# Optimization experiments

Measured on AMD Instinct MI355X. Metric: run time of the kernel, lower is better.

Reference implementation:

```python
import jax, jax.numpy as jnp
import numpy as np

# dims
B, S, D, H, F = 4, 1024, 1024, 16, 4096
DH = D // H
THETA0 = 1.0   # base firing threshold of AdaptiveLIFNeuron
RHO = 0.9      # adaptation decay
EPS = 1e-5


def layer_norm(x, g, b):
    mu = jnp.mean(x, axis=-1, keepdims=True)
    var = jnp.mean((x - mu) ** 2, axis=-1, keepdims=True)
    return (x - mu) * jax.lax.rsqrt(var + EPS) * g + b


def spike(u):
    # Heaviside forward, sigmoid surrogate gradient (straight-through)
    sg = jax.nn.sigmoid(4.0 * u)
    hard = (u > 0).astype(u.dtype)
    return sg + jax.lax.stop_gradient(hard - sg)


def setup_inputs() -> dict:
    key = jax.random.key(0)
    ks = jax.random.split(key, 8)
    std = 0.02
    w = lambda k, shape: jax.random.normal(k, shape, jnp.float32) * std
    return {
        "x": jax.random.normal(ks[0], (B, S, D), jnp.float32),
        "Wq": w(ks[1], (D, D)), "bq": jnp.zeros((D,), jnp.float32),
        "Wk": w(ks[2], (D, D)), "bk": jnp.zeros((D,), jnp.float32),
        "Wv": w(ks[3], (D, D)), "bv": jnp.zeros((D,), jnp.float32),
        "Wo": w(ks[4], (D, D)), "bo": jnp.zeros((D,), jnp.float32),
        "g1": jnp.ones((D,), jnp.float32), "b1": jnp.zeros((D,), jnp.float32),
        "W1": w(ks[5], (D, F)), "bf1": jnp.zeros((F,), jnp.float32),
        "W2": w(ks[6], (F, D)), "bf2": jnp.zeros((D,), jnp.float32),
        "g2": jnp.ones((D,), jnp.float32), "b2": jnp.zeros((D,), jnp.float32),
        "decay": jnp.full((F,), 0.8, jnp.float32),  # per-feature membrane leak
        "beta": jnp.full((F,), 0.1, jnp.float32),   # per-feature threshold adaptation
    }


def reference(x, Wq, bq, Wk, bk, Wv, bv, Wo, bo, g1, b1, W1, bf1, W2, bf2, g2, b2, decay, beta):
    # --- causal multi-head self-attention (DSALayer) ---
    q = (x @ Wq + bq).reshape(B, S, H, DH)
    k = (x @ Wk + bk).reshape(B, S, H, DH)
    v = (x @ Wv + bv).reshape(B, S, H, DH)
    scores = jnp.einsum("bqhd,bkhd->bhqk", q, k) / np.sqrt(DH).astype(np.float32)
    causal = jnp.tril(jnp.ones((S, S), bool))
    scores = jnp.where(causal, scores, jnp.asarray(-1e9, scores.dtype))
    p = jax.nn.softmax(scores, axis=-1)
    attn = jnp.einsum("bhqk,bkhd->bqhd", p, v).reshape(B, S, D) @ Wo + bo
    h = layer_norm(x + attn, g1, b1)

    # --- feed-forward with per-timestep adaptive LIF recurrence ---
    ff = h @ W1 + bf1                      # [B, S, F]

    def step(carry, xt):
        vm, a = carry                      # membrane potential, adaptation
        vm = decay * vm + xt
        u = vm - (THETA0 + a)
        s = spike(u)
        vm = vm * (1.0 - s)                # hard reset on spike
        a = RHO * a + beta * s
        return (vm, a), s

    init = (jnp.zeros((B, F), x.dtype), jnp.zeros((B, F), x.dtype))
    _, spikes = jax.lax.scan(step, init, jnp.swapaxes(ff, 0, 1))  # scan over time
    spikes = jnp.swapaxes(spikes, 0, 1)    # [B, S, F]

    ff_out = spikes @ W2 + bf2
    return layer_norm(h + ff_out, g2, b2)
```

## Files before the change

### kernel.cpp

```cpp
#include <hip/hip_runtime.h>
#include <hip/hip_bf16.h>
#include <stdint.h>

#define Bsz 4
#define Ssz 1024
#define Dsz 1024
#define Hsz 16
#define Fsz 4096

typedef __hip_bfloat16 bf16;
typedef __attribute__((ext_vector_type(8))) short bf16x8;
typedef __attribute__((ext_vector_type(4))) float f32x4;

typedef __attribute__((address_space(1))) const void gvoid_t;
typedef __attribute__((address_space(3))) void svoid_t;

__device__ __forceinline__ void gload16(const bf16* g, bf16* l) {
    __builtin_amdgcn_global_load_lds((gvoid_t*)g, (svoid_t*)l, 16, 0, 0);
}

__global__ __launch_bounds__(256) void split_k(const float* __restrict__ src,
                                               bf16* __restrict__ hi,
                                               bf16* __restrict__ lo) {
    const int i = (blockIdx.x * 256 + threadIdx.x) * 4;
    const float4 v = *(const float4*)(src + i);
    float vv[4] = {v.x, v.y, v.z, v.w};
    #pragma unroll
    for (int u = 0; u < 4; ++u) {
        const bf16 h = __float2bfloat16(vv[u]);
        hi[i + u] = h;
        lo[i + u] = __float2bfloat16(vv[u] - __bfloat162float(h));
    }
}

__global__ __launch_bounds__(256) void split_scale_strided_k(const float* __restrict__ src,
                                                             int stride, int coloff,
                                                             bf16* __restrict__ hi,
                                                             bf16* __restrict__ lo,
                                                             float scale) {
    const int i = (blockIdx.x * 256 + threadIdx.x) * 4;
    const int r = i >> 10, c = i & 1023;
    const float4 v = *(const float4*)(src + (size_t)r * stride + coloff + c);
    float vv[4] = {v.x * scale, v.y * scale, v.z * scale, v.w * scale};
    #pragma unroll
    for (int u = 0; u < 4; ++u) {
        const bf16 h = __float2bfloat16(vv[u]);
        hi[i + u] = h;
        lo[i + u] = __float2bfloat16(vv[u] - __bfloat162float(h));
    }
}

__global__ __launch_bounds__(256) void transpose_split_k(const float* __restrict__ in,
                                                         bf16* __restrict__ hiT,
                                                         bf16* __restrict__ loT,
                                                         int R, int C) {
    __shared__ float tile[32][33];
    const int bx = blockIdx.x * 32, by = blockIdx.y * 32;
    const int tx = threadIdx.x, ty = threadIdx.y;
    #pragma unroll
    for (int i = 0; i < 32; i += 8)
        tile[ty + i][tx] = in[(size_t)(by + ty + i) * C + bx + tx];
    __syncthreads();
    #pragma unroll
    for (int i = 0; i < 32; i += 8) {
        const float v = tile[tx][ty + i];
        const bf16 h = __float2bfloat16(v);
        const size_t o = (size_t)(bx + ty + i) * R + by + tx;
        hiT[o] = h;
        loT[o] = __float2bfloat16(v - __bfloat162float(h));
    }
}

__global__ __launch_bounds__(256) void transpose_cast_k(const float* __restrict__ in,
                                                        bf16* __restrict__ outT,
                                                        int R, int C) {
    __shared__ float tile[32][33];
    const int bx = blockIdx.x * 32, by = blockIdx.y * 32;
    const int tx = threadIdx.x, ty = threadIdx.y;
    #pragma unroll
    for (int i = 0; i < 32; i += 8)
        tile[ty + i][tx] = in[(size_t)(by + ty + i) * C + bx + tx];
    __syncthreads();
    #pragma unroll
    for (int i = 0; i < 32; i += 8)
        outT[(size_t)(bx + ty + i) * R + by + tx] = __float2bfloat16(tile[tx][ty + i]);
}

__global__ __launch_bounds__(256) void transpose_split_v_k(const float* __restrict__ v,
                                                           int stride, int coloff,
                                                           bf16* __restrict__ hiT,
                                                           bf16* __restrict__ loT) {
    __shared__ float tile[32][33];
    const int s0 = blockIdx.x * 32;
    const int dr0 = blockIdx.y * 32;
    const int b = dr0 >> 10, h = (dr0 >> 6) & 15, d0 = dr0 & 63;
    const int tx = threadIdx.x, ty = threadIdx.y;
    #pragma unroll
    for (int i = 0; i < 32; i += 8)
        tile[ty + i][tx] =
            v[(size_t)(b * Ssz + s0 + ty + i) * stride + coloff + h * 64 + d0 + tx];
    __syncthreads();
    #pragma unroll
    for (int i = 0; i < 32; i += 8) {
        const float val = tile[tx][ty + i];
        const bf16 hh = __float2bfloat16(val);
        const size_t o = (size_t)(dr0 + ty + i) * Ssz + s0 + tx;
        hiT[o] = hh;
        loT[o] = __float2bfloat16(val - __bfloat162float(hh));
    }
}

__global__ __launch_bounds__(256) void gemm3_bt(const bf16* __restrict__ Ah,
                                                const bf16* __restrict__ Al,
                                                const bf16* __restrict__ Bh,
                                                const bf16* __restrict__ Bl,
                                                const float* __restrict__ bias,
                                                float* __restrict__ Cf,
                                                int M, int N, int K) {
    __shared__ alignas(16) bf16 Ash[128 * 32];
    __shared__ alignas(16) bf16 Asl[128 * 32];
    __shared__ alignas(16) bf16 Bsh[128 * 32];
    __shared__ alignas(16) bf16 Bsl[128 * 32];
    const int t = threadIdx.x;
    const int lane = t & 63, wv = t >> 6;
    const int mw = wv >> 1, nw = wv & 1;
    const int m0 = blockIdx.y * 128, n0 = blockIdx.x * 128;
    const int r16 = lane & 15, q8 = (lane >> 4) * 8;
    const int arow = t >> 2, acol = (t & 3) * 8;

    const bf16* gAh = Ah + (size_t)(m0 + arow) * K + acol;
    const bf16* gAl = Al + (size_t)(m0 + arow) * K + acol;
    const bf16* gBh = Bh + (size_t)(n0 + arow) * K + acol;
    const bf16* gBl = Bl + (size_t)(n0 + arow) * K + acol;
    const size_t rK64 = (size_t)64 * K;
    bf16* lAh = Ash + wv * 512;
    bf16* lAl = Asl + wv * 512;
    bf16* lBh = Bsh + wv * 512;
    bf16* lBl = Bsl + wv * 512;

    f32x4 acc[4][4] = {};

    for (int k0 = 0; k0 < K; k0 += 32) {
        __syncthreads();
        gload16(gAh + k0, lAh);  gload16(gAh + k0 + rK64, lAh + 2048);
        gload16(gAl + k0, lAl);  gload16(gAl + k0 + rK64, lAl + 2048);
        gload16(gBh + k0, lBh);  gload16(gBh + k0 + rK64, lBh + 2048);
        gload16(gBl + k0, lBl);  gload16(gBl + k0 + rK64, lBl + 2048);
        __syncthreads();

        bf16x8 ah[4], al[4], bh[4], bl[4];
        #pragma unroll
        for (int rt = 0; rt < 4; ++rt) {
            const int ro = (64 * mw + 16 * rt + r16) * 32 + q8;
            ah[rt] = *(const bf16x8*)(Ash + ro);
            al[rt] = *(const bf16x8*)(Asl + ro);
        }
        #pragma unroll
        for (int ct = 0; ct < 4; ++ct) {
            const int co = (64 * nw + 16 * ct + r16) * 32 + q8;
            bh[ct] = *(const bf16x8*)(Bsh + co);
            bl[ct] = *(const bf16x8*)(Bsl + co);
        }
        #pragma unroll
        for (int rt = 0; rt < 4; ++rt)
            #pragma unroll
            for (int ct = 0; ct < 4; ++ct) {
                acc[rt][ct] = __builtin_amdgcn_mfma_f32_16x16x32_bf16(ah[rt], bh[ct], acc[rt][ct], 0, 0, 0);
                acc[rt][ct] = __builtin_amdgcn_mfma_f32_16x16x32_bf16(ah[rt], bl[ct], acc[rt][ct], 0, 0, 0);
                acc[rt][ct] = __builtin_amdgcn_mfma_f32_16x16x32_bf16(al[rt], bh[ct], acc[rt][ct], 0, 0, 0);
            }
    }

    const int rowi = (lane >> 4) * 4;
    const int coli = lane & 15;
    #pragma unroll
    for (int ct = 0; ct < 4; ++ct) {
        const int col = n0 + 64 * nw + 16 * ct + coli;
        const float bv = bias[col];
        #pragma unroll
        for (int rt = 0; rt < 4; ++rt) {
            const int rowb = m0 + 64 * mw + 16 * rt + rowi;
            #pragma unroll
            for (int r = 0; r < 4; ++r)
                Cf[(size_t)(rowb + r) * N + col] = acc[rt][ct][r] + bv;
        }
    }
}

__global__ __launch_bounds__(256) void gemm1_bt(const bf16* __restrict__ A,
                                                const bf16* __restrict__ Bt,
                                                const float* __restrict__ bias,
                                                float* __restrict__ Cf,
                                                int M, int N, int K) {
    __shared__ alignas(16) bf16 As[128 * 32];
    __shared__ alignas(16) bf16 Bs[128 * 32];
    const int t = threadIdx.x;
    const int lane = t & 63, wv = t >> 6;
    const int mw = wv >> 1, nw = wv & 1;
    const int m0 = blockIdx.y * 128, n0 = blockIdx.x * 128;
    const int r16 = lane & 15, q8 = (lane >> 4) * 8;
    const int arow = t >> 2, acol = (t & 3) * 8;

    const bf16* gA = A + (size_t)(m0 + arow) * K + acol;
    const bf16* gB = Bt + (size_t)(n0 + arow) * K + acol;
    const size_t rK64 = (size_t)64 * K;
    bf16* lA = As + wv * 512;
    bf16* lB = Bs + wv * 512;

    f32x4 acc[4][4] = {};

    for (int k0 = 0; k0 < K; k0 += 32) {
        __syncthreads();
        gload16(gA + k0, lA);  gload16(gA + k0 + rK64, lA + 2048);
        gload16(gB + k0, lB);  gload16(gB + k0 + rK64, lB + 2048);
        __syncthreads();

        bf16x8 af[4], bf_[4];
        #pragma unroll
        for (int rt = 0; rt < 4; ++rt)
            af[rt] = *(const bf16x8*)(As + (64 * mw + 16 * rt + r16) * 32 + q8);
        #pragma unroll
        for (int ct = 0; ct < 4; ++ct)
            bf_[ct] = *(const bf16x8*)(Bs + (64 * nw + 16 * ct + r16) * 32 + q8);
        #pragma unroll
        for (int rt = 0; rt < 4; ++rt)
            #pragma unroll
            for (int ct = 0; ct < 4; ++ct)
                acc[rt][ct] = __builtin_amdgcn_mfma_f32_16x16x32_bf16(
                    af[rt], bf_[ct], acc[rt][ct], 0, 0, 0);
    }

    const int rowi = (lane >> 4) * 4;
    const int coli = lane & 15;
    #pragma unroll
    for (int ct = 0; ct < 4; ++ct) {
        const int col = n0 + 64 * nw + 16 * ct + coli;
        const float bv = bias[col];
        #pragma unroll
        for (int rt = 0; rt < 4; ++rt) {
            const int rowb = m0 + 64 * mw + 16 * rt + rowi;
            #pragma unroll
            for (int r = 0; r < 4; ++r)
                Cf[(size_t)(rowb + r) * N + col] = acc[rt][ct][r] + bv;
        }
    }
}

__global__ __launch_bounds__(256) void attn_mfma_k(const bf16* __restrict__ qhp,
                                                   const bf16* __restrict__ qlp,
                                                   const bf16* __restrict__ khp,
                                                   const bf16* __restrict__ klp,
                                                   const bf16* __restrict__ vhp,
                                                   const bf16* __restrict__ vlp,
                                                   bf16* __restrict__ ohi,
                                                   bf16* __restrict__ olo) {
    __shared__ alignas(16) bf16 Qh[64 * 72], Ql[64 * 72];
    __shared__ alignas(16) bf16 Kh[64 * 72], Kl[64 * 72];
    __shared__ alignas(16) bf16 Vh[64 * 72], Vl[64 * 72];
    __shared__ alignas(16) bf16 Ph[64 * 72], Pl[64 * 72];

    const int bh = blockIdx.y;
    const int b = bh >> 4, h = bh & 15;
    const int q0 = (gridDim.x - 1 - blockIdx.x) * 64;
    const int t = threadIdx.x, w = t >> 6, lane = t & 63;
    const int r16 = lane & 15, quad = lane >> 4;
    const int sr = t >> 2, sc = (t & 3) * 16;

    {
        const size_t g = (size_t)(b * Ssz + q0 + sr) * Dsz + h * 64 + sc;
        *(uint4*)&Qh[sr * 72 + sc]     = *(const uint4*)(qhp + g);
        *(uint4*)&Qh[sr * 72 + sc + 8] = *(const uint4*)(qhp + g + 8);
        *(uint4*)&Ql[sr * 72 + sc]     = *(const uint4*)(qlp + g);
        *(uint4*)&Ql[sr * 72 + sc + 8] = *(const uint4*)(qlp + g + 8);
    }

    f32x4 aco[4] = {};
    float lrun[4] = {0.f, 0.f, 0.f, 0.f};
    const int ntiles = q0 / 64 + 1;

    for (int kt = 0; kt < ntiles; ++kt) {
        __syncthreads();
        {
            const size_t g = (size_t)(b * Ssz + kt * 64 + sr) * Dsz + h * 64 + sc;
            *(uint4*)&Kh[sr * 72 + sc]     = *(const uint4*)(khp + g);
            *(uint4*)&Kh[sr * 72 + sc + 8] = *(const uint4*)(khp + g + 8);
            *(uint4*)&Kl[sr * 72 + sc]     = *(const uint4*)(klp + g);
            *(uint4*)&Kl[sr * 72 + sc + 8] = *(const uint4*)(klp + g + 8);
            const size_t gv = ((size_t)bh * 64 + sr) * Ssz + kt * 64 + sc;
            *(uint4*)&Vh[sr * 72 + sc]     = *(const uint4*)(vhp + gv);
            *(uint4*)&Vh[sr * 72 + sc + 8] = *(const uint4*)(vhp + gv + 8);
            *(uint4*)&Vl[sr * 72 + sc]     = *(const uint4*)(vlp + gv);
            *(uint4*)&Vl[sr * 72 + sc + 8] = *(const uint4*)(vlp + gv + 8);
        }
        __syncthreads();

        bf16x8 aQh[2], aQl[2];
        #pragma unroll
        for (int ks = 0; ks < 2; ++ks) {
            aQh[ks] = *(const bf16x8*)&Qh[(16 * w + r16) * 72 + ks * 32 + quad * 8];
            aQl[ks] = *(const bf16x8*)&Ql[(16 * w + r16) * 72 + ks * 32 + quad * 8];
        }
        #pragma unroll
        for (int nt = 0; nt < 4; ++nt) {
            f32x4 s = {};
            #pragma unroll
            for (int ks = 0; ks < 2; ++ks) {
                const bf16x8 bKh = *(const bf16x8*)&Kh[(16 * nt + r16) * 72 + ks * 32 + quad * 8];
                const bf16x8 bKl = *(const bf16x8*)&Kl[(16 * nt + r16) * 72 + ks * 32 + quad * 8];
                s = __builtin_amdgcn_mfma_f32_16x16x32_bf16(aQh[ks], bKh, s, 0, 0, 0);
                s = __builtin_amdgcn_mfma_f32_16x16x32_bf16(aQh[ks], bKl, s, 0, 0, 0);
                s = __builtin_amdgcn_mfma_f32_16x16x32_bf16(aQl[ks], bKh, s, 0, 0, 0);
            }
            const int key = kt * 64 + nt * 16 + r16;
            #pragma unroll
            for (int r = 0; r < 4; ++r) {
                const int qrow = q0 + 16 * w + quad * 4 + r;
                const float p = (key <= qrow) ? __expf(s[r]) : 0.f;
                lrun[r] += p;
                const bf16 ph = __float2bfloat16(p);
                Ph[(16 * w + quad * 4 + r) * 72 + nt * 16 + r16] = ph;
                Pl[(16 * w + quad * 4 + r) * 72 + nt * 16 + r16] =
                    __float2bfloat16(p - __bfloat162float(ph));
            }
        }

        bf16x8 aPh[2], aPl[2];
        #pragma unroll
        for (int ks = 0; ks < 2; ++ks) {
            aPh[ks] = *(const bf16x8*)&Ph[(16 * w + r16) * 72 + ks * 32 + quad * 8];
            aPl[ks] = *(const bf16x8*)&Pl[(16 * w + r16) * 72 + ks * 32 + quad * 8];
        }
        #pragma unroll
        for (int nt = 0; nt < 4; ++nt) {
            #pragma unroll
            for (int ks = 0; ks < 2; ++ks) {
                const bf16x8 bVh = *(const bf16x8*)&Vh[(16 * nt + r16) * 72 + ks * 32 + quad * 8];
                const bf16x8 bVl = *(const bf16x8*)&Vl[(16 * nt + r16) * 72 + ks * 32 + quad * 8];
                aco[nt] = __builtin_amdgcn_mfma_f32_16x16x32_bf16(aPh[ks], bVh, aco[nt], 0, 0, 0);
                aco[nt] = __builtin_amdgcn_mfma_f32_16x16x32_bf16(aPh[ks], bVl, aco[nt], 0, 0, 0);
                aco[nt] = __builtin_amdgcn_mfma_f32_16x16x32_bf16(aPl[ks], bVh, aco[nt], 0, 0, 0);
            }
        }
    }

    #pragma unroll
    for (int r = 0; r < 4; ++r) {
        float l = lrun[r];
        l += __shfl_xor(l, 1); l += __shfl_xor(l, 2);
        l += __shfl_xor(l, 4); l += __shfl_xor(l, 8);
        lrun[r] = l;
    }
    #pragma unroll
    for (int nt = 0; nt < 4; ++nt)
        #pragma unroll
        for (int r = 0; r < 4; ++r) {
            const size_t off = (size_t)(b * Ssz + q0 + 16 * w + quad * 4 + r) * Dsz
                               + h * 64 + nt * 16 + r16;
            const float val = aco[nt][r] / lrun[r];
            const bf16 hh = __float2bfloat16(val);
            ohi[off] = hh;
            olo[off] = __float2bfloat16(val - __bfloat162float(hh));
        }
}

__global__ __launch_bounds__(64) void scan_k(const float* __restrict__ ff,
                                             const float* __restrict__ decay,
                                             const float* __restrict__ beta,
                                             bf16* __restrict__ spikes) {
    const int idx = blockIdx.x * 64 + threadIdx.x;
    const int b = idx >> 12;
    const int f = idx & (Fsz - 1);
    const float dec = decay[f];
    const float bet = beta[f];
    const float* src = ff + (size_t)b * Ssz * Fsz + f;
    bf16* dst = spikes + (size_t)b * Ssz * Fsz + f;
    float vm = 0.f, a = 0.f;
    float buf[8], nbuf[8];
    #pragma unroll
    for (int u = 0; u < 8; ++u) buf[u] = src[(size_t)u * Fsz];
    for (int t0 = 0; t0 < Ssz; t0 += 8) {
        const bool more = (t0 + 8) < Ssz;
        #pragma unroll
        for (int u = 0; u < 8; ++u)
            nbuf[u] = more ? src[(size_t)(t0 + 8 + u) * Fsz] : 0.f;
        #pragma unroll
        for (int u = 0; u < 8; ++u) {
            vm = dec * vm + buf[u];
            const float uu = vm - (1.f + a);
            const float sp = (uu > 0.f) ? 1.f : 0.f;
            vm = (uu > 0.f) ? 0.f : vm;
            a = 0.9f * a + bet * sp;
            dst[(size_t)(t0 + u) * Fsz] = __float2bfloat16(sp);
        }
        #pragma unroll
        for (int u = 0; u < 8; ++u) buf[u] = nbuf[u];
    }
}

__device__ __forceinline__ float block_sum(float val, float* ls, int t) {
    #pragma unroll
    for (int mm = 32; mm >= 1; mm >>= 1) val += __shfl_xor(val, mm);
    if ((t & 63) == 0) ls[t >> 6] = val;
    __syncthreads();
    const float r = ls[0] + ls[1] + ls[2] + ls[3];
    __syncthreads();
    return r;
}

__global__ __launch_bounds__(256) void ln1_k(const float* __restrict__ x,
                                             const float* __restrict__ ap,
                                             const float* __restrict__ g,
                                             const float* __restrict__ bb,
                                             bf16* __restrict__ h_hi,
                                             bf16* __restrict__ h_lo) {
    __shared__ float ls[4];
    const int row = blockIdx.x;
    const int t = threadIdx.x;
    const size_t base = (size_t)row * Dsz;
    float vv[4];
    #pragma unroll
    for (int i = 0; i < 4; ++i) {
        const int c = t + i * 256;
        vv[i] = x[base + c] + ap[base + c];
    }
    float s = vv[0] + vv[1] + vv[2] + vv[3];
    s = block_sum(s, ls, t);
    const float mu = s * (1.f / 1024.f);
    float qs = 0.f;
    #pragma unroll
    for (int i = 0; i < 4; ++i) { const float d = vv[i] - mu; qs += d * d; }
    qs = block_sum(qs, ls, t);
    const float rs = rsqrtf(qs * (1.f / 1024.f) + 1e-5f);
    #pragma unroll
    for (int i = 0; i < 4; ++i) {
        const int c = t + i * 256;
        const float o = (vv[i] - mu) * rs * g[c] + bb[c];
        const bf16 hi = __float2bfloat16(o);
        h_hi[base + c] = hi;
        h_lo[base + c] = __float2bfloat16(o - __bfloat162float(hi));
    }
}

__global__ __launch_bounds__(256) void ln2_k(const bf16* __restrict__ h_hi,
                                             const bf16* __restrict__ h_lo,
                                             const float* __restrict__ fo,
                                             const float* __restrict__ g,
                                             const float* __restrict__ bb,
                                             float* __restrict__ out) {
    __shared__ float ls[4];
    const int row = blockIdx.x;
    const int t = threadIdx.x;
    const size_t base = (size_t)row * Dsz;
    float vv[4];
    #pragma unroll
    for (int i = 0; i < 4; ++i) {
        const int c = t + i * 256;
        const float h = __bfloat162float(h_hi[base + c]) + __bfloat162float(h_lo[base + c]);
        vv[i] = h + fo[base + c];
    }
    float s = vv[0] + vv[1] + vv[2] + vv[3];
    s = block_sum(s, ls, t);
    const float mu = s * (1.f / 1024.f);
    float qs = 0.f;
    #pragma unroll
    for (int i = 0; i < 4; ++i) { const float d = vv[i] - mu; qs += d * d; }
    qs = block_sum(qs, ls, t);
    const float rs = rsqrtf(qs * (1.f / 1024.f) + 1e-5f);
    #pragma unroll
    for (int i = 0; i < 4; ++i) {
        const int c = t + i * 256;
        out[base + c] = (vv[i] - mu) * rs * g[c] + bb[c];
    }
}

extern "C" void kernel_launch(void* const* d_in, const int* in_sizes, int n_in,
                              void* d_out, int out_size, void* d_ws, size_t ws_size,
                              hipStream_t stream) {
    const float* x    = (const float*)d_in[0];
    const float* Wq   = (const float*)d_in[1];
    const float* bq   = (const float*)d_in[2];
    const float* Wk   = (const float*)d_in[3];
    const float* bk   = (const float*)d_in[4];
    const float* Wv   = (const float*)d_in[5];
    const float* bv   = (const float*)d_in[6];
    const float* Wo   = (const float*)d_in[7];
    const float* bo   = (const float*)d_in[8];
    const float* g1   = (const float*)d_in[9];
    const float* b1   = (const float*)d_in[10];
    const float* W1   = (const float*)d_in[11];
    const float* bf1  = (const float*)d_in[12];
    const float* W2   = (const float*)d_in[13];
    const float* bf2  = (const float*)d_in[14];
    const float* g2   = (const float*)d_in[15];
    const float* b2   = (const float*)d_in[16];
    const float* dec  = (const float*)d_in[17];
    const float* beta = (const float*)d_in[18];

    const size_t BSD = (size_t)Bsz * Ssz * Dsz;
    const size_t BSF = (size_t)Bsz * Ssz * Fsz;

    char* ws = (char*)d_ws;
    char* A3 = ws;
    char* A1 = A3 + BSF * 4;
    char* A2 = A1 + BSF * 2;
    char* A4 = A2 + (size_t)Dsz * Fsz * 2 * 2;
    float* bqkv = (float*)(A4 + BSD * 4);

    float* qkvf  = (float*)(A3);
    float* attnp = (float*)(A3 + (size_t)Bsz * Ssz * 3072 * 4);
    float* ffb   = (float*)(A3);
    float* ffout = (float*)(A3);

    bf16* xhi    = (bf16*)(A1);
    bf16* xlo    = (bf16*)(A1 + BSD * 2);
    bf16* qhi    = (bf16*)(A1);
    bf16* qlo    = (bf16*)(A1 + BSD * 2);
    bf16* khi    = (bf16*)(A1 + BSD * 4);
    bf16* klo    = (bf16*)(A1 + BSD * 6);
    bf16* athi   = (bf16*)(A1);
    bf16* atlo   = (bf16*)(A1 + BSD * 2);
    bf16* spikes = (bf16*)(A1);

    const size_t WP = (size_t)Dsz * Dsz;
    bf16* Wqkv_hi = (bf16*)(A2);
    bf16* Wqkv_lo = (bf16*)(A2 + WP * 3 * 2);
    bf16* WoThi   = (bf16*)(A2 + WP * 6 * 2);
    bf16* WoTlo   = (bf16*)(A2 + WP * 7 * 2);
    bf16* W1Thi   = (bf16*)(A2);
    bf16* W1Tlo   = (bf16*)(A2 + (size_t)Dsz * Fsz * 2);
    bf16* W2T     = (bf16*)(A2);

    bf16* vthi  = (bf16*)(A4);
    bf16* vtlo  = (bf16*)(A4 + BSD * 2);
    bf16* h_hi  = (bf16*)(A4);
    bf16* h_lo  = (bf16*)(A4 + BSD * 2);

    (void)ws_size; (void)in_sizes; (void)n_in; (void)out_size;

    const dim3 tb(32, 8);
    const int MBS = Bsz * Ssz;

    split_k<<<BSD / 1024, 256, 0, stream>>>(x, xhi, xlo);
    transpose_split_k<<<dim3(32, 32), tb, 0, stream>>>(Wq, Wqkv_hi, Wqkv_lo, Dsz, Dsz);
    transpose_split_k<<<dim3(32, 32), tb, 0, stream>>>(Wk, Wqkv_hi + WP, Wqkv_lo + WP, Dsz, Dsz);
    transpose_split_k<<<dim3(32, 32), tb, 0, stream>>>(Wv, Wqkv_hi + WP * 2, Wqkv_lo + WP * 2, Dsz, Dsz);
    transpose_split_k<<<dim3(32, 32), tb, 0, stream>>>(Wo, WoThi, WoTlo, Dsz, Dsz);
    hipMemcpyAsync(bqkv,        (const void*)bq, Dsz * 4, hipMemcpyDeviceToDevice, stream);
    hipMemcpyAsync(bqkv + 1024, (const void*)bk, Dsz * 4, hipMemcpyDeviceToDevice, stream);
    hipMemcpyAsync(bqkv + 2048, (const void*)bv, Dsz * 4, hipMemcpyDeviceToDevice, stream);

    gemm3_bt<<<dim3(3072 / 128, MBS / 128), 256, 0, stream>>>(
        xhi, xlo, Wqkv_hi, Wqkv_lo, bqkv, qkvf, MBS, 3072, Dsz);

    split_scale_strided_k<<<BSD / 1024, 256, 0, stream>>>(qkvf, 3072, 0, qhi, qlo, 0.125f);
    split_scale_strided_k<<<BSD / 1024, 256, 0, stream>>>(qkvf, 3072, 1024, khi, klo, 1.0f);
    transpose_split_v_k<<<dim3(Ssz / 32, Bsz * Hsz * 64 / 32), tb, 0, stream>>>(
        qkvf, 3072, 2048, vthi, vtlo);
    attn_mfma_k<<<dim3(Ssz / 64, Bsz * Hsz), 256, 0, stream>>>(
        qhi, qlo, khi, klo, vthi, vtlo, athi, atlo);

    gemm3_bt<<<dim3(Dsz / 128, MBS / 128), 256, 0, stream>>>(
        athi, atlo, WoThi, WoTlo, bo, attnp, MBS, Dsz, Dsz);
    ln1_k<<<MBS, 256, 0, stream>>>(x, attnp, g1, b1, h_hi, h_lo);

    transpose_split_k<<<dim3(Fsz / 32, Dsz / 32), tb, 0, stream>>>(W1, W1Thi, W1Tlo, Dsz, Fsz);
    gemm3_bt<<<dim3(Fsz / 128, MBS / 128), 256, 0, stream>>>(
        h_hi, h_lo, W1Thi, W1Tlo, bf1, ffb, MBS, Fsz, Dsz);

    scan_k<<<Bsz * Fsz / 64, 64, 0, stream>>>(ffb, dec, beta, spikes);

    transpose_cast_k<<<dim3(Dsz / 32, Fsz / 32), tb, 0, stream>>>(W2, W2T, Fsz, Dsz);
    gemm1_bt<<<dim3(Dsz / 128, MBS / 128), 256, 0, stream>>>(
        spikes, W2T, bf2, ffout, MBS, Dsz, Fsz);

    ln2_k<<<MBS, 256, 0, stream>>>(h_hi, h_lo, ffout, g2, b2, (float*)d_out);
}
```

Measured before the change: 685.4 us.

## Fuse QKV split/scale/transpose into GEMM epilogue; batch weight transposes; deepen scan prefetch

The QKV GEMM now writes bf16 hi/lo Q (pre-scaled), K, and transposed V directly from its epilogue. This removes the fp32 qkv intermediate and three separate split/transpose kernels. The four weight transposes are merged into one launch using blockIdx.z. The LIF scan kernel now prefetches 64 timesteps into registers in rotating 16-step groups, which raises register pressure. The V epilogue stores 4 strided values per lane as 8-byte writes, which may coalesce less well than the old transpose kernel.

```diff
diff --git a/kernel.cpp b/kernel.cpp
--- a/kernel.cpp
+++ b/kernel.cpp
@@ -33,20 +33,33 @@
     }
 }
 
-__global__ __launch_bounds__(256) void split_scale_strided_k(const float* __restrict__ src,
-                                                             int stride, int coloff,
-                                                             bf16* __restrict__ hi,
-                                                             bf16* __restrict__ lo,
-                                                             float scale) {
-    const int i = (blockIdx.x * 256 + threadIdx.x) * 4;
-    const int r = i >> 10, c = i & 1023;
-    const float4 v = *(const float4*)(src + (size_t)r * stride + coloff + c);
-    float vv[4] = {v.x * scale, v.y * scale, v.z * scale, v.w * scale};
-    #pragma unroll
-    for (int u = 0; u < 4; ++u) {
-        const bf16 h = __float2bfloat16(vv[u]);
-        hi[i + u] = h;
-        lo[i + u] = __float2bfloat16(vv[u] - __bfloat162float(h));
+__global__ __launch_bounds__(256) void transpose_split4_k(const float* __restrict__ Wq,
+                                                          const float* __restrict__ Wk,
+                                                          const float* __restrict__ Wv,
+                                                          const float* __restrict__ Wo,
+                                                          bf16* __restrict__ qkv_hi,
+                                                          bf16* __restrict__ qkv_lo,
+                                                          bf16* __restrict__ wo_hi,
+                                                          bf16* __restrict__ wo_lo) {
+    __shared__ float tile[32][33];
+    const int z = blockIdx.z;
+    const float* in = (z == 0) ? Wq : (z == 1) ? Wk : (z == 2) ? Wv : Wo;
+    const size_t WP = (size_t)Dsz * Dsz;
+    bf16* hiT = (z < 3) ? qkv_hi + (size_t)z * WP : wo_hi;
+    bf16* loT = (z < 3) ? qkv_lo + (size_t)z * WP : wo_lo;
+    const int bx = blockIdx.x * 32, by = blockIdx.y * 32;
+    const int tx = threadIdx.x, ty = threadIdx.y;
+    #pragma unroll
+    for (int i = 0; i < 32; i += 8)
+        tile[ty + i][tx] = in[(size_t)(by + ty + i) * Dsz + bx + tx];
+    __syncthreads();
+    #pragma unroll
+    for (int i = 0; i < 32; i += 8) {
+        const float v = tile[tx][ty + i];
+        const bf16 h = __float2bfloat16(v);
+        const size_t o = (size_t)(bx + ty + i) * Dsz + by + tx;
+        hiT[o] = h;
+        loT[o] = __float2bfloat16(v - __bfloat162float(h));
     }
 }
 
@@ -84,30 +97,6 @@
     #pragma unroll
     for (int i = 0; i < 32; i += 8)
         outT[(size_t)(bx + ty + i) * R + by + tx] = __float2bfloat16(tile[tx][ty + i]);
-}
-
-__global__ __launch_bounds__(256) void transpose_split_v_k(const float* __restrict__ v,
-                                                           int stride, int coloff,
-                                                           bf16* __restrict__ hiT,
-                                                           bf16* __restrict__ loT) {
-    __shared__ float tile[32][33];
-    const int s0 = blockIdx.x * 32;
-    const int dr0 = blockIdx.y * 32;
-    const int b = dr0 >> 10, h = (dr0 >> 6) & 15, d0 = dr0 & 63;
-    const int tx = threadIdx.x, ty = threadIdx.y;
-    #pragma unroll
-    for (int i = 0; i < 32; i += 8)
-        tile[ty + i][tx] =
-            v[(size_t)(b * Ssz + s0 + ty + i) * stride + coloff + h * 64 + d0 + tx];
-    __syncthreads();
-    #pragma unroll
-    for (int i = 0; i < 32; i += 8) {
-        const float val = tile[tx][ty + i];
-        const bf16 hh = __float2bfloat16(val);
-        const size_t o = (size_t)(dr0 + ty + i) * Ssz + s0 + tx;
-        hiT[o] = hh;
-        loT[o] = __float2bfloat16(val - __bfloat162float(hh));
-    }
 }
 
 __global__ __launch_bounds__(256) void gemm3_bt(const bf16* __restrict__ Ah,
@@ -187,6 +176,120 @@
     }
 }
 
+__global__ __launch_bounds__(256) void gemm3_qkv(const bf16* __restrict__ Ah,
+                                                 const bf16* __restrict__ Al,
+                                                 const bf16* __restrict__ Bh,
+                                                 const bf16* __restrict__ Bl,
+                                                 const float* __restrict__ bias,
+                                                 bf16* __restrict__ qhi, bf16* __restrict__ qlo,
+                                                 bf16* __restrict__ khi, bf16* __restrict__ klo,
+                                                 bf16* __restrict__ vthi, bf16* __restrict__ vtlo) {
+    const int K = Dsz;
+    __shared__ alignas(16) bf16 Ash[128 * 32];
+    __shared__ alignas(16) bf16 Asl[128 * 32];
+    __shared__ alignas(16) bf16 Bsh[128 * 32];
+    __shared__ alignas(16) bf16 Bsl[128 * 32];
+    const int t = threadIdx.x;
+    const int lane = t & 63, wv = t >> 6;
+    const int mw = wv >> 1, nw = wv & 1;
+    const int m0 = blockIdx.y * 128, n0 = blockIdx.x * 128;
+    const int r16 = lane & 15, q8 = (lane >> 4) * 8;
+    const int arow = t >> 2, acol = (t & 3) * 8;
+
+    const bf16* gAh = Ah + (size_t)(m0 + arow) * K + acol;
+    const bf16* gAl = Al + (size_t)(m0 + arow) * K + acol;
+    const bf16* gBh = Bh + (size_t)(n0 + arow) * K + acol;
+    const bf16* gBl = Bl + (size_t)(n0 + arow) * K + acol;
+    const size_t rK64 = (size_t)64 * K;
+    bf16* lAh = Ash + wv * 512;
+    bf16* lAl = Asl + wv * 512;
+    bf16* lBh = Bsh + wv * 512;
+    bf16* lBl = Bsl + wv * 512;
+
+    f32x4 acc[4][4] = {};
+
+    for (int k0 = 0; k0 < K; k0 += 32) {
+        __syncthreads();
+        gload16(gAh + k0, lAh);  gload16(gAh + k0 + rK64, lAh + 2048);
+        gload16(gAl + k0, lAl);  gload16(gAl + k0 + rK64, lAl + 2048);
+        gload16(gBh + k0, lBh);  gload16(gBh + k0 + rK64, lBh + 2048);
+        gload16(gBl + k0, lBl);  gload16(gBl + k0 + rK64, lBl + 2048);
+        __syncthreads();
+
+        bf16x8 ah[4], al[4], bh[4], bl[4];
+        #pragma unroll
+        for (int rt = 0; rt < 4; ++rt) {
+            const int ro = (64 * mw + 16 * rt + r16) * 32 + q8;
+            ah[rt] = *(const bf16x8*)(Ash + ro);
+            al[rt] = *(const bf16x8*)(Asl + ro);
+        }
+        #pragma unroll
+        for (int ct = 0; ct < 4; ++ct) {
+            const int co = (64 * nw + 16 * ct + r16) * 32 + q8;
+            bh[ct] = *(const bf16x8*)(Bsh + co);
+            bl[ct] = *(const bf16x8*)(Bsl + co);
+        }
+        #pragma unroll
+        for (int rt = 0; rt < 4; ++rt)
+            #pragma unroll
+            for (int ct = 0; ct < 4; ++ct) {
+                acc[rt][ct] = __builtin_amdgcn_mfma_f32_16x16x32_bf16(ah[rt], bh[ct], acc[rt][ct], 0, 0, 0);
+                acc[rt][ct] = __builtin_amdgcn_mfma_f32_16x16x32_bf16(ah[rt], bl[ct], acc[rt][ct], 0, 0, 0);
+                acc[rt][ct] = __builtin_amdgcn_mfma_f32_16x16x32_bf16(al[rt], bh[ct], acc[rt][ct], 0, 0, 0);
+            }
+    }
+
+    const int rowi = (lane >> 4) * 4;
+    const int coli = lane & 15;
+    if (n0 < 2048) {
+        const float scale = (n0 < 1024) ? 0.125f : 1.0f;
+        bf16* hip_ = (n0 < 1024) ? qhi : khi;
+        bf16* lop_ = (n0 < 1024) ? qlo : klo;
+        const int cbase = (n0 < 1024) ? n0 : (n0 - 1024);
+        #pragma unroll
+        for (int ct = 0; ct < 4; ++ct) {
+            const int col = cbase + 64 * nw + 16 * ct + coli;
+            const float bv = bias[n0 + 64 * nw + 16 * ct + coli];
+            #pragma unroll
+            for (int rt = 0; rt < 4; ++rt) {
+                const int rowb = m0 + 64 * mw + 16 * rt + rowi;
+                #pragma unroll
+                for (int r = 0; r < 4; ++r) {
+                    const float val = (acc[rt][ct][r] + bv) * scale;
+                    const bf16 h = __float2bfloat16(val);
+                    const size_t off = (size_t)(rowb + r) * Dsz + col;
+                    hip_[off] = h;
+                    lop_[off] = __float2bfloat16(val - __bfloat162float(h));
+                }
+            }
+        }
+    } else {
+        #pragma unroll
+        for (int ct = 0; ct < 4; ++ct) {
+            const int col = n0 + 64 * nw + 16 * ct + coli;
+            const float bv = bias[col];
+            const int c2 = col - 2048;
+            #pragma unroll
+            for (int rt = 0; rt < 4; ++rt) {
+                const int rowb = m0 + 64 * mw + 16 * rt + rowi;
+                const int b = rowb >> 10, s = rowb & 1023;
+                const size_t off = ((size_t)b * 16384 + (size_t)c2 * 1024) + s + 65536 * 0;
+                bf16 hv[4], lv[4];
+                #pragma unroll
+                for (int r = 0; r < 4; ++r) {
+                    const float val = acc[rt][ct][r] + bv;
+                    hv[r] = __float2bfloat16(val);
+                    lv[r] = __float2bfloat16(val - __bfloat162float(hv[r]));
+                }
+                const size_t vo = (size_t)b * (16 * 64 * 1024) + (size_t)c2 * 1024 + s;
+                (void)off;
+                *(uint2*)&vthi[vo] = *(const uint2*)hv;
+                *(uint2*)&vtlo[vo] = *(const uint2*)lv;
+            }
+        }
+    }
+}
+
 __global__ __launch_bounds__(256) void gemm1_bt(const bf16* __restrict__ A,
                                                 const bf16* __restrict__ Bt,
                                                 const float* __restrict__ bias,
@@ -375,25 +478,28 @@
     const float* src = ff + (size_t)b * Ssz * Fsz + f;
     bf16* dst = spikes + (size_t)b * Ssz * Fsz + f;
     float vm = 0.f, a = 0.f;
-    float buf[8], nbuf[8];
-    #pragma unroll
-    for (int u = 0; u < 8; ++u) buf[u] = src[(size_t)u * Fsz];
-    for (int t0 = 0; t0 < Ssz; t0 += 8) {
-        const bool more = (t0 + 8) < Ssz;
-        #pragma unroll
-        for (int u = 0; u < 8; ++u)
-            nbuf[u] = more ? src[(size_t)(t0 + 8 + u) * Fsz] : 0.f;
-        #pragma unroll
-        for (int u = 0; u < 8; ++u) {
-            vm = dec * vm + buf[u];
-            const float uu = vm - (1.f + a);
-            const float sp = (uu > 0.f) ? 1.f : 0.f;
-            vm = (uu > 0.f) ? 0.f : vm;
-            a = 0.9f * a + bet * sp;
-            dst[(size_t)(t0 + u) * Fsz] = __float2bfloat16(sp);
-        }
-        #pragma unroll
-        for (int u = 0; u < 8; ++u) buf[u] = nbuf[u];
+    float buf[64];
+    #pragma unroll
+    for (int u = 0; u < 64; ++u) buf[u] = src[(size_t)u * Fsz];
+    for (int gg = 0; gg < 16; ++gg) {
+        #pragma unroll
+        for (int sub = 0; sub < 4; ++sub) {
+            const int g = gg * 4 + sub;
+            #pragma unroll
+            for (int u = 0; u < 16; ++u) {
+                vm = dec * vm + buf[sub * 16 + u];
+                const float uu = vm - (1.f + a);
+                const float sp = (uu > 0.f) ? 1.f : 0.f;
+                vm = (uu > 0.f) ? 0.f : vm;
+                a = 0.9f * a + bet * sp;
+                dst[(size_t)(g * 16 + u) * Fsz] = __float2bfloat16(sp);
+            }
+            if (g + 4 < 64) {
+                #pragma unroll
+                for (int u = 0; u < 16; ++u)
+                    buf[sub * 16 + u] = src[(size_t)((g + 4) * 16 + u) * Fsz];
+            }
+        }
     }
 }
 
@@ -506,17 +612,16 @@
     char* A4 = A2 + (size_t)Dsz * Fsz * 2 * 2;
     float* bqkv = (float*)(A4 + BSD * 4);
 
-    float* qkvf  = (float*)(A3);
-    float* attnp = (float*)(A3 + (size_t)Bsz * Ssz * 3072 * 4);
+    bf16* qhi   = (bf16*)(A3);
+    bf16* qlo   = (bf16*)(A3 + BSD * 2);
+    bf16* khi   = (bf16*)(A3 + BSD * 4);
+    bf16* klo   = (bf16*)(A3 + BSD * 6);
+    float* attnp = (float*)(A3 + BSD * 12);
     float* ffb   = (float*)(A3);
     float* ffout = (float*)(A3);
 
     bf16* xhi    = (bf16*)(A1);
     bf16* xlo    = (bf16*)(A1 + BSD * 2);
-    bf16* qhi    = (bf16*)(A1);
-    bf16* qlo    = (bf16*)(A1 + BSD * 2);
-    bf16* khi    = (bf16*)(A1 + BSD * 4);
-    bf16* klo    = (bf16*)(A1 + BSD * 6);
     bf16* athi   = (bf16*)(A1);
     bf16* atlo   = (bf16*)(A1 + BSD * 2);
     bf16* spikes = (bf16*)(A1);
@@ -541,21 +646,15 @@
     const int MBS = Bsz * Ssz;
 
     split_k<<<BSD / 1024, 256, 0, stream>>>(x, xhi, xlo);
-    transpose_split_k<<<dim3(32, 32), tb, 0, stream>>>(Wq, Wqkv_hi, Wqkv_lo, Dsz, Dsz);
-    transpose_split_k<<<dim3(32, 32), tb, 0, stream>>>(Wk, Wqkv_hi + WP, Wqkv_lo + WP, Dsz, Dsz);
-    transpose_split_k<<<dim3(32, 32), tb, 0, stream>>>(Wv, Wqkv_hi + WP * 2, Wqkv_lo + WP * 2, Dsz, Dsz);
-    transpose_split_k<<<dim3(32, 32), tb, 0, stream>>>(Wo, WoThi, WoTlo, Dsz, Dsz);
+    transpose_split4_k<<<dim3(32, 32, 4), tb, 0, stream>>>(
+        Wq, Wk, Wv, Wo, Wqkv_hi, Wqkv_lo, WoThi, WoTlo);
     hipMemcpyAsync(bqkv,        (const void*)bq, Dsz * 4, hipMemcpyDeviceToDevice, stream);
     hipMemcpyAsync(bqkv + 1024, (const void*)bk, Dsz * 4, hipMemcpyDeviceToDevice, stream);
     hipMemcpyAsync(bqkv + 2048, (const void*)bv, Dsz * 4, hipMemcpyDeviceToDevice, stream);
 
-    gemm3_bt<<<dim3(3072 / 128, MBS / 128), 256, 0, stream>>>(
-        xhi, xlo, Wqkv_hi, Wqkv_lo, bqkv, qkvf, MBS, 3072, Dsz);
-
-    split_scale_strided_k<<<BSD / 1024, 256, 0, stream>>>(qkvf, 3072, 0, qhi, qlo, 0.125f);
-    split_scale_strided_k<<<BSD / 1024, 256, 0, stream>>>(qkvf, 3072, 1024, khi, klo, 1.0f);
-    transpose_split_v_k<<<dim3(Ssz / 32, Bsz * Hsz * 64 / 32), tb, 0, stream>>>(
-        qkvf, 3072, 2048, vthi, vtlo);
+    gemm3_qkv<<<dim3(3072 / 128, MBS / 128), 256, 0, stream>>>(
+        xhi, xlo, Wqkv_hi, Wqkv_lo, bqkv, qhi, qlo, khi, klo, vthi, vtlo);
+
     attn_mfma_k<<<dim3(Ssz / 64, Bsz * Hsz), 256, 0, stream>>>(
         qhi, qlo, khi, klo, vthi, vtlo, athi, atlo);
 
```

New measurement: 644.9 us. 5.9% less time.
